# Performance work log

Measured on AMD Instinct MI355X. Metric: run time of the kernel, lower is better.

Reference implementation:

```python
import jax, jax.numpy as jnp
import numpy as np

N = 50000
E = 600000
D_IN = 128
HID = 128
OUT = 64


def setup_inputs() -> dict:
    key = jax.random.key(0)
    ks = jax.random.split(key, 12)
    x = jax.random.normal(ks[0], (N, D_IN), dtype=jnp.float32)
    edge_index = jax.random.randint(ks[1], (2, E), 0, N, dtype=jnp.int32)
    def lin(k, fan_in, fan_out):
        lim = 1.0 / np.sqrt(fan_in)
        kw, kb = jax.random.split(k)
        W = jax.random.uniform(kw, (fan_in, fan_out), minval=-lim, maxval=lim, dtype=jnp.float32)
        b = jax.random.uniform(kb, (fan_out,), minval=-lim, maxval=lim, dtype=jnp.float32)
        return W, b
    W1, b1 = lin(ks[2], D_IN, HID)
    W2, b2 = lin(ks[3], HID, HID)
    W3, b3 = lin(ks[4], HID, HID)
    fcW, fcb = lin(ks[5], HID, OUT)
    return {"x": x, "edge_index": edge_index, "W1": W1, "b1": b1,
            "W2": W2, "b2": b2, "W3": W3, "b3": b3, "fcW": fcW, "fcb": fcb}


def _gcn_prep(edge_index):
    # add self loops, compute symmetric normalization deg^-1/2 * deg^-1/2
    loop = jnp.arange(N, dtype=edge_index.dtype)
    src = jnp.concatenate([edge_index[0], loop])
    dst = jnp.concatenate([edge_index[1], loop])
    deg = jax.ops.segment_sum(jnp.ones_like(dst, dtype=jnp.float32), dst, num_segments=N)
    dinv = jnp.where(deg > 0, jax.lax.rsqrt(deg), 0.0)
    norm = dinv[src] * dinv[dst]  # [E+N]
    return src, dst, norm


def _gcn_layer(x, src, dst, norm, W, b):
    h = x @ W                      # [N, F_out]
    msg = h[src] * norm[:, None]   # gather + scale, [E+N, F_out]
    agg = jax.ops.segment_sum(msg, dst, num_segments=N)
    return agg + b


def reference(x, edge_index, W1, b1, W2, b2, W3, b3, fcW, fcb):
    src, dst, norm = _gcn_prep(edge_index)
    x = jax.nn.relu(_gcn_layer(x, src, dst, norm, W1, b1))
    x = jax.nn.relu(_gcn_layer(x, src, dst, norm, W2, b2))
    x = jax.nn.relu(_gcn_layer(x, src, dst, norm, W3, b3))
    virtual_node_embedding = x[-1]  # last node's embedding [HID]
    out = virtual_node_embedding @ fcW + fcb  # [OUT]
    return out
```

## Files before the change

kernel.cpp:

```cpp
#include <hip/hip_runtime.h>

#define NF 128
#define OUTF 64

#define M2 1
#define M1 2
#define M0 4

#define CAP_F2 2048
#define CAP_E3 4096
#define CAP_F1 32768
#define CAP_E2 65536
#define CAP_F0 131072
#define CAP_E1 262144


__global__ void k_seed(int* __restrict__ mark, int* __restrict__ F2,
                       int* __restrict__ cnt, int last) {
    if (threadIdx.x == 0) {
        mark[last] = M2;
        F2[0] = last;
        cnt[0] = 1;
    }
}

__global__ void k_mark(const int* __restrict__ src, const int* __restrict__ dst, int E,
                       int* __restrict__ mark, int checkBit, int setBit, int last,
                       int2* __restrict__ Elist, int Ecap, int* __restrict__ eCnt,
                       int* __restrict__ Flist, int Fcap, int* __restrict__ fCnt,
                       const int* __restrict__ selfList, const int* __restrict__ selfCnt,
                       int selfCap)
{
    int i = blockIdx.x * blockDim.x + threadIdx.x;

    if (selfList) {
        int sc = *selfCnt; if (sc > selfCap) sc = selfCap;
        if (i < sc) {
            int v = selfList[i];
            if (!(atomicOr(&mark[v], setBit) & setBit)) {
                int p = atomicAdd(fCnt, 1);
                if (p < Fcap) Flist[p] = v;
            }
        }
    }
    if (i < E) {
        int d = dst[i];
        bool hit = checkBit ? ((mark[d] & checkBit) != 0) : (d == last);
        if (hit) {
            int s = src[i];
            int p = atomicAdd(eCnt, 1);
            if (p < Ecap) Elist[p] = make_int2(s, d);
            if (!(atomicOr(&mark[s], setBit) & setBit)) {
                int q = atomicAdd(fCnt, 1);
                if (q < Fcap) Flist[q] = s;
            }
        }
    }
}

__global__ void k_degm(const int* __restrict__ dst, const int* __restrict__ mark,
                       int* __restrict__ deg, int E) {
    int i = blockIdx.x * blockDim.x + threadIdx.x;
    if (i < E) {
        int d = dst[i];
        if (mark[d]) atomicAdd(&deg[d], 1);
    }
}

__global__ void k_dinvm(const int* __restrict__ mark, const int* __restrict__ deg,
                        float* __restrict__ dinv, int n) {
    int i = blockIdx.x * blockDim.x + threadIdx.x;
    if (i < n && mark[i]) dinv[i] = rsqrtf(1.0f + (float)deg[i]);
}

__global__ __launch_bounds__(256) void k_gemm_rows(
    const int* __restrict__ list, const int* __restrict__ cntPtr, int cap,
    const float* __restrict__ Xin, const float* __restrict__ bias,
    const float* __restrict__ W, const float* __restrict__ dinv,
    const int* __restrict__ mark, int aggBit, int last,
    float* __restrict__ H, float* __restrict__ AGG)
{
    __shared__ float wsm[128][128];
    const int t = threadIdx.x;

    {
        const float4* W4 = (const float4*)W;
        float4* S4 = (float4*)&wsm[0][0];
        #pragma unroll
        for (int it = 0; it < 16; ++it) S4[it * 256 + t] = W4[it * 256 + t];
    }
    __syncthreads();

    int cnt = *cntPtr; if (cnt > cap) cnt = cap;
    const int wave = t >> 6, lane = t & 63;

    for (int base = blockIdx.x * 4; base < cnt; base += gridDim.x * 4) {
        int r = base + wave;
        if (r >= cnt) continue;
        int v = list[r];
        size_t off = (size_t)v * NF;

        float x0, x1;
        if (bias) {
            x0 = fmaxf(Xin[off + lane]      + bias[lane],      0.f);
            x1 = fmaxf(Xin[off + lane + 64] + bias[lane + 64], 0.f);
        } else {
            x0 = Xin[off + lane];
            x1 = Xin[off + lane + 64];
        }

        float a0 = 0.f, a1 = 0.f;
        #pragma unroll 16
        for (int k = 0; k < 64; ++k) {
            float xk = __shfl(x0, k);
            a0 += xk * wsm[k][lane];
            a1 += xk * wsm[k][lane + 64];
        }
        #pragma unroll 16
        for (int k = 0; k < 64; ++k) {
            float xk = __shfl(x1, k);
            a0 += xk * wsm[k + 64][lane];
            a1 += xk * wsm[k + 64][lane + 64];
        }

        H[off + lane]      = a0;
        H[off + lane + 64] = a1;

        bool doAgg = (mark ? ((mark[v] & aggBit) != 0) : false) || (v == last);
        if (doAgg) {
            float di = dinv[v], s2 = di * di;
            AGG[off + lane]      = a0 * s2;
            AGG[off + lane + 64] = a1 * s2;
        }
    }
}

__global__ void k_scat(const int2* __restrict__ list, const int* __restrict__ cntPtr, int cap,
                       const float* __restrict__ dinv, const float* __restrict__ H,
                       float* __restrict__ AGG)
{
    int cnt = *cntPtr; if (cnt > cap) cnt = cap;
    int t = threadIdx.x;
    for (int i = blockIdx.x; i < cnt; i += gridDim.x) {
        int2 e = list[i];
        float w = dinv[e.x] * dinv[e.y];
        atomicAdd(&AGG[(size_t)e.y * NF + t], H[(size_t)e.x * NF + t] * w);
    }
}

__global__ void k_fc(const float* __restrict__ AGG3, const float* __restrict__ b3,
                     const float* __restrict__ fcW, const float* __restrict__ fcb,
                     float* __restrict__ out, int last)
{
    __shared__ float xrow[NF];
    int j = threadIdx.x;
    size_t off = (size_t)last * NF;
    xrow[j]      = fmaxf(AGG3[off + j]      + b3[j],      0.f);
    xrow[j + 64] = fmaxf(AGG3[off + j + 64] + b3[j + 64], 0.f);
    __syncthreads();
    float acc = fcb[j];
    #pragma unroll 16
    for (int k = 0; k < NF; ++k) acc += xrow[k] * fcW[k * OUTF + j];
    out[j] = acc;
}

extern "C" void kernel_launch(void* const* d_in, const int* in_sizes, int n_in,
                              void* d_out, int out_size, void* d_ws, size_t ws_size,
                              hipStream_t stream)
{
    const float* x    = (const float*)d_in[0];
    const int*   ei   = (const int*)d_in[1];
    const float* W1   = (const float*)d_in[2];
    const float* b1   = (const float*)d_in[3];
    const float* W2   = (const float*)d_in[4];
    const float* b2   = (const float*)d_in[5];
    const float* W3   = (const float*)d_in[6];
    const float* b3   = (const float*)d_in[7];
    const float* fcW  = (const float*)d_in[8];
    const float* fcb  = (const float*)d_in[9];
    float* out = (float*)d_out;

    const int n = in_sizes[0] / NF;
    const int E = in_sizes[1] / 2;
    const int* src = ei;
    const int* dst = ei + E;
    const int last = n - 1;

    char* wp = (char*)d_ws;
    auto alloc = [&](size_t bytes) -> void* {
        void* r = (void*)wp;
        wp += (bytes + 255) & ~(size_t)255;
        return r;
    };
    int*   deg  = (int*)alloc((size_t)n * 4);
    int*   mark = (int*)alloc((size_t)n * 4);
    int*   cnt  = (int*)alloc(64 * 4);
    size_t zbytes = (char*)wp - (char*)deg;

    float* dinv = (float*)alloc((size_t)n * 4);
    int*   F2   = (int*) alloc(CAP_F2 * 4);
    int2*  E3   = (int2*)alloc(CAP_E3 * 8);
    int*   F1   = (int*) alloc(CAP_F1 * 4);
    int2*  E2   = (int2*)alloc(CAP_E2 * 8);
    int*   F0   = (int*) alloc(CAP_F0 * 4);
    int2*  E1   = (int2*)alloc(CAP_E1 * 8);
    float* H    = (float*)alloc((size_t)n * NF * 4);
    float* aggA = (float*)alloc((size_t)n * NF * 4);
    float* aggB = (float*)alloc((size_t)n * NF * 4);

    const int B  = 256;
    const int EB = (E + B - 1) / B;
    const int NB = (n + B - 1) / B;

    hipMemsetAsync(deg, 0, zbytes, stream);
    k_seed<<<1, 64, 0, stream>>>(mark, F2, cnt, last);

    k_mark<<<EB, B, 0, stream>>>(src, dst, E, mark, 0,  M2, last,
                                 E3, CAP_E3, &cnt[1], F2, CAP_F2, &cnt[0],
                                 nullptr, nullptr, 0);
    k_mark<<<EB, B, 0, stream>>>(src, dst, E, mark, M2, M1, last,
                                 E2, CAP_E2, &cnt[3], F1, CAP_F1, &cnt[2],
                                 F2, &cnt[0], CAP_F2);
    k_mark<<<EB, B, 0, stream>>>(src, dst, E, mark, M1, M0, last,
                                 E1, CAP_E1, &cnt[5], F0, CAP_F0, &cnt[4],
                                 F1, &cnt[2], CAP_F1);

    k_degm <<<EB, B, 0, stream>>>(dst, mark, deg, E);
    k_dinvm<<<NB, B, 0, stream>>>(mark, deg, dinv, n);

    k_gemm_rows<<<384, B, 0, stream>>>(F0, &cnt[4], CAP_F0, x, nullptr, W1,
                                       dinv, mark, M1, -1, H, aggA);
    k_scat<<<2048, 128, 0, stream>>>(E1, &cnt[5], CAP_E1, dinv, H, aggA);

    k_gemm_rows<<<384, B, 0, stream>>>(F1, &cnt[2], CAP_F1, aggA, b1, W2,
                                       dinv, mark, M2, -1, H, aggB);
    k_scat<<<2048, 128, 0, stream>>>(E2, &cnt[3], CAP_E2, dinv, H, aggB);

    k_gemm_rows<<<384, B, 0, stream>>>(F2, &cnt[0], CAP_F2, aggB, b2, W3,
                                       dinv, nullptr, 0, last, H, aggA);
    k_scat<<<2048, 128, 0, stream>>>(E3, &cnt[1], CAP_E3, dinv, H, aggA);

    k_fc<<<1, 64, 0, stream>>>(aggA, b3, fcW, fcb, out, last);
}
```

Measured before the change: 167.8 us.

## Fuse all GCN stages into one cooperative persistent kernel with grid syncs

Replaces about twelve separate launches (memset, seed, three mark passes, degree, dinv, three gemm and scatter pairs, fc) with a single cooperative kernel of 256 blocks that separates phases with grid.sync. Degree counting is folded into the first edge pass and dinv is recomputed on the fly from deg instead of being stored. The aim is to remove launch overhead and inter-kernel gaps. In exchange, parallelism is capped at 256 blocks, every phase pays a grid-wide barrier, and degree atomics now run for all edges rather than only marked destinations.

```diff
diff --git a/kernel.cpp b/kernel.cpp
--- a/kernel.cpp
+++ b/kernel.cpp
@@ -1,4 +1,7 @@
 #include <hip/hip_runtime.h>
+#include <hip/hip_cooperative_groups.h>
+
+namespace cg = cooperative_groups;
 
 #define NF 128
 #define OUTF 64
@@ -15,176 +18,201 @@
 #define CAP_E1 262144
 
 
-__global__ void k_seed(int* __restrict__ mark, int* __restrict__ F2,
-                       int* __restrict__ cnt, int last) {
-    if (threadIdx.x == 0) {
-        mark[last] = M2;
-        F2[0] = last;
-        cnt[0] = 1;
-    }
+struct Params {
+    const float* x; const int* src; const int* dst; int E; int n; int last;
+    const float* W1; const float* b1; const float* W2; const float* b2;
+    const float* W3; const float* b3; const float* fcW; const float* fcb;
+    int* deg; int* mark; int* cnt;
+    int* F2; int2* E3l; int* F1; int2* E2l; int* F0; int2* E1l;
+    float* H; float* aggA; float* aggB; float* out;
+};
+
+__device__ __forceinline__ float dinv_of(const int* deg, int v) {
+    return rsqrtf(1.0f + (float)deg[v]);
 }
 
-__global__ void k_mark(const int* __restrict__ src, const int* __restrict__ dst, int E,
-                       int* __restrict__ mark, int checkBit, int setBit, int last,
-                       int2* __restrict__ Elist, int Ecap, int* __restrict__ eCnt,
-                       int* __restrict__ Flist, int Fcap, int* __restrict__ fCnt,
-                       const int* __restrict__ selfList, const int* __restrict__ selfCnt,
-                       int selfCap)
-{
-    int i = blockIdx.x * blockDim.x + threadIdx.x;
-
-    if (selfList) {
-        int sc = *selfCnt; if (sc > selfCap) sc = selfCap;
-        if (i < sc) {
-            int v = selfList[i];
-            if (!(atomicOr(&mark[v], setBit) & setBit)) {
-                int p = atomicAdd(fCnt, 1);
-                if (p < Fcap) Flist[p] = v;
-            }
-        }
-    }
-    if (i < E) {
-        int d = dst[i];
-        bool hit = checkBit ? ((mark[d] & checkBit) != 0) : (d == last);
-        if (hit) {
-            int s = src[i];
-            int p = atomicAdd(eCnt, 1);
-            if (p < Ecap) Elist[p] = make_int2(s, d);
-            if (!(atomicOr(&mark[s], setBit) & setBit)) {
-                int q = atomicAdd(fCnt, 1);
-                if (q < Fcap) Flist[q] = s;
-            }
-        }
-    }
-}
-
-__global__ void k_degm(const int* __restrict__ dst, const int* __restrict__ mark,
-                       int* __restrict__ deg, int E) {
-    int i = blockIdx.x * blockDim.x + threadIdx.x;
-    if (i < E) {
-        int d = dst[i];
-        if (mark[d]) atomicAdd(&deg[d], 1);
-    }
-}
-
-__global__ void k_dinvm(const int* __restrict__ mark, const int* __restrict__ deg,
-                        float* __restrict__ dinv, int n) {
-    int i = blockIdx.x * blockDim.x + threadIdx.x;
-    if (i < n && mark[i]) dinv[i] = rsqrtf(1.0f + (float)deg[i]);
-}
-
-__global__ __launch_bounds__(256) void k_gemm_rows(
-    const int* __restrict__ list, const int* __restrict__ cntPtr, int cap,
-    const float* __restrict__ Xin, const float* __restrict__ bias,
-    const float* __restrict__ W, const float* __restrict__ dinv,
-    const int* __restrict__ mark, int aggBit, int last,
-    float* __restrict__ H, float* __restrict__ AGG)
-{
+__global__ __launch_bounds__(256) void k_fused(Params p) {
+    cg::grid_group grid = cg::this_grid();
     __shared__ float wsm[128][128];
-    const int t = threadIdx.x;
+
+    const int t       = threadIdx.x;
+    const int gtid    = blockIdx.x * 256 + t;
+    const int gstride = gridDim.x * 256;
+    const int last    = p.last;
+
+    for (int i = gtid; i < p.n; i += gstride) {
+        p.deg[i]  = 0;
+        p.mark[i] = (i == last) ? M2 : 0;
+    }
+    if (gtid < 64) p.cnt[gtid] = (gtid == 0) ? 1 : 0;
+    if (gtid == 0) p.F2[0] = last;
+    grid.sync();
+
+    for (int i = gtid; i < p.E; i += gstride) {
+        int d = p.dst[i];
+        atomicAdd(&p.deg[d], 1);
+        if (d == last) {
+            int s = p.src[i];
+            int pe = atomicAdd(&p.cnt[1], 1);
+            if (pe < CAP_E3) p.E3l[pe] = make_int2(s, d);
+            if (!(atomicOr(&p.mark[s], M2) & M2)) {
+                int q = atomicAdd(&p.cnt[0], 1);
+                if (q < CAP_F2) p.F2[q] = s;
+            }
+        }
+    }
+    grid.sync();
 
     {
-        const float4* W4 = (const float4*)W;
+        int sc = p.cnt[0]; if (sc > CAP_F2) sc = CAP_F2;
+        for (int i = gtid; i < sc; i += gstride) {
+            int v = p.F2[i];
+            if (!(atomicOr(&p.mark[v], M1) & M1)) {
+                int q = atomicAdd(&p.cnt[2], 1);
+                if (q < CAP_F1) p.F1[q] = v;
+            }
+        }
+        for (int i = gtid; i < p.E; i += gstride) {
+            int d = p.dst[i];
+            if (p.mark[d] & M2) {
+                int s = p.src[i];
+                int pe = atomicAdd(&p.cnt[3], 1);
+                if (pe < CAP_E2) p.E2l[pe] = make_int2(s, d);
+                if (!(atomicOr(&p.mark[s], M1) & M1)) {
+                    int q = atomicAdd(&p.cnt[2], 1);
+                    if (q < CAP_F1) p.F1[q] = s;
+                }
+            }
+        }
+    }
+    grid.sync();
+
+    {
+        int sc = p.cnt[2]; if (sc > CAP_F1) sc = CAP_F1;
+        for (int i = gtid; i < sc; i += gstride) {
+            int v = p.F1[i];
+            if (!(atomicOr(&p.mark[v], M0) & M0)) {
+                int q = atomicAdd(&p.cnt[4], 1);
+                if (q < CAP_F0) p.F0[q] = v;
+            }
+        }
+        for (int i = gtid; i < p.E; i += gstride) {
+            int d = p.dst[i];
+            if (p.mark[d] & M1) {
+                int s = p.src[i];
+                int pe = atomicAdd(&p.cnt[5], 1);
+                if (pe < CAP_E1) p.E1l[pe] = make_int2(s, d);
+                if (!(atomicOr(&p.mark[s], M0) & M0)) {
+                    int q = atomicAdd(&p.cnt[4], 1);
+                    if (q < CAP_F0) p.F0[q] = s;
+                }
+            }
+        }
+    }
+    grid.sync();
+
+    int cF2 = p.cnt[0]; if (cF2 > CAP_F2) cF2 = CAP_F2;
+    int cE3 = p.cnt[1]; if (cE3 > CAP_E3) cE3 = CAP_E3;
+    int cF1 = p.cnt[2]; if (cF1 > CAP_F1) cF1 = CAP_F1;
+    int cE2 = p.cnt[3]; if (cE2 > CAP_E2) cE2 = CAP_E2;
+    int cF0 = p.cnt[4]; if (cF0 > CAP_F0) cF0 = CAP_F0;
+    int cE1 = p.cnt[5]; if (cE1 > CAP_E1) cE1 = CAP_E1;
+
+    const int wave = t >> 6, lane = t & 63;
+
+    auto gemm = [&](const int* list, int cntv, const float* Xin, const float* bias,
+                    const float* Wg, int aggBit, float* H, float* AGG) {
+        const float4* W4 = (const float4*)Wg;
         float4* S4 = (float4*)&wsm[0][0];
         #pragma unroll
         for (int it = 0; it < 16; ++it) S4[it * 256 + t] = W4[it * 256 + t];
-    }
-    __syncthreads();
-
-    int cnt = *cntPtr; if (cnt > cap) cnt = cap;
-    const int wave = t >> 6, lane = t & 63;
-
-    for (int base = blockIdx.x * 4; base < cnt; base += gridDim.x * 4) {
-        int r = base + wave;
-        if (r >= cnt) continue;
-        int v = list[r];
-        size_t off = (size_t)v * NF;
-
-        float x0, x1;
-        if (bias) {
-            x0 = fmaxf(Xin[off + lane]      + bias[lane],      0.f);
-            x1 = fmaxf(Xin[off + lane + 64] + bias[lane + 64], 0.f);
-        } else {
-            x0 = Xin[off + lane];
-            x1 = Xin[off + lane + 64];
-        }
-
-        float a0 = 0.f, a1 = 0.f;
-        #pragma unroll 16
-        for (int k = 0; k < 64; ++k) {
-            float xk = __shfl(x0, k);
-            a0 += xk * wsm[k][lane];
-            a1 += xk * wsm[k][lane + 64];
-        }
-        #pragma unroll 16
-        for (int k = 0; k < 64; ++k) {
-            float xk = __shfl(x1, k);
-            a0 += xk * wsm[k + 64][lane];
-            a1 += xk * wsm[k + 64][lane + 64];
-        }
-
-        H[off + lane]      = a0;
-        H[off + lane + 64] = a1;
-
-        bool doAgg = (mark ? ((mark[v] & aggBit) != 0) : false) || (v == last);
-        if (doAgg) {
-            float di = dinv[v], s2 = di * di;
-            AGG[off + lane]      = a0 * s2;
-            AGG[off + lane + 64] = a1 * s2;
-        }
-    }
-}
-
-__global__ void k_scat(const int2* __restrict__ list, const int* __restrict__ cntPtr, int cap,
-                       const float* __restrict__ dinv, const float* __restrict__ H,
-                       float* __restrict__ AGG)
-{
-    int cnt = *cntPtr; if (cnt > cap) cnt = cap;
-    int t = threadIdx.x;
-    for (int i = blockIdx.x; i < cnt; i += gridDim.x) {
-        int2 e = list[i];
-        float w = dinv[e.x] * dinv[e.y];
-        atomicAdd(&AGG[(size_t)e.y * NF + t], H[(size_t)e.x * NF + t] * w);
-    }
-}
-
-__global__ void k_fc(const float* __restrict__ AGG3, const float* __restrict__ b3,
-                     const float* __restrict__ fcW, const float* __restrict__ fcb,
-                     float* __restrict__ out, int last)
-{
-    __shared__ float xrow[NF];
-    int j = threadIdx.x;
-    size_t off = (size_t)last * NF;
-    xrow[j]      = fmaxf(AGG3[off + j]      + b3[j],      0.f);
-    xrow[j + 64] = fmaxf(AGG3[off + j + 64] + b3[j + 64], 0.f);
-    __syncthreads();
-    float acc = fcb[j];
-    #pragma unroll 16
-    for (int k = 0; k < NF; ++k) acc += xrow[k] * fcW[k * OUTF + j];
-    out[j] = acc;
+        __syncthreads();
+
+        for (int r = blockIdx.x * 4 + wave; r < cntv; r += gridDim.x * 4) {
+            int v = list[r];
+            size_t off = (size_t)v * NF;
+            float x0, x1;
+            if (bias) {
+                x0 = fmaxf(Xin[off + lane]      + bias[lane],      0.f);
+                x1 = fmaxf(Xin[off + lane + 64] + bias[lane + 64], 0.f);
+            } else {
+                x0 = Xin[off + lane];
+                x1 = Xin[off + lane + 64];
+            }
+            float a0 = 0.f, a1 = 0.f;
+            #pragma unroll 16
+            for (int k = 0; k < 64; ++k) {
+                float xk = __shfl(x0, k);
+                a0 += xk * wsm[k][lane];
+                a1 += xk * wsm[k][lane + 64];
+            }
+            #pragma unroll 16
+            for (int k = 0; k < 64; ++k) {
+                float xk = __shfl(x1, k);
+                a0 += xk * wsm[k + 64][lane];
+                a1 += xk * wsm[k + 64][lane + 64];
+            }
+            H[off + lane]      = a0;
+            H[off + lane + 64] = a1;
+
+            bool doAgg = aggBit ? ((p.mark[v] & aggBit) != 0) : (v == last);
+            if (doAgg) {
+                float di = dinv_of(p.deg, v);
+                float s2 = di * di;
+                AGG[off + lane]      = a0 * s2;
+                AGG[off + lane + 64] = a1 * s2;
+            }
+        }
+    };
+
+    auto scat = [&](const int2* El, int ec, const float* H, float* AGG) {
+        int half = t >> 7;
+        int f    = t & 127;
+        for (int i = blockIdx.x * 2 + half; i < ec; i += gridDim.x * 2) {
+            int2 e = El[i];
+            float w = dinv_of(p.deg, e.x) * dinv_of(p.deg, e.y);
+            atomicAdd(&AGG[(size_t)e.y * NF + f], H[(size_t)e.x * NF + f] * w);
+        }
+    };
+
+    gemm(p.F0, cF0, p.x, nullptr, p.W1, M1, p.H, p.aggA);
+    grid.sync();
+    scat(p.E1l, cE1, p.H, p.aggA);
+    grid.sync();
+
+    gemm(p.F1, cF1, p.aggA, p.b1, p.W2, M2, p.H, p.aggB);
+    grid.sync();
+    scat(p.E2l, cE2, p.H, p.aggB);
+    grid.sync();
+
+    gemm(p.F2, cF2, p.aggB, p.b2, p.W3, 0, p.H, p.aggA);
+    grid.sync();
+    scat(p.E3l, cE3, p.H, p.aggA);
+    grid.sync();
+
+    if (blockIdx.x == 0) {
+        float* xrow = &wsm[0][0];
+        size_t off = (size_t)last * NF;
+        if (t < 64) {
+            xrow[t]      = fmaxf(p.aggA[off + t]      + p.b3[t],      0.f);
+            xrow[t + 64] = fmaxf(p.aggA[off + t + 64] + p.b3[t + 64], 0.f);
+        }
+        __syncthreads();
+        if (t < 64) {
+            float acc = p.fcb[t];
+            #pragma unroll 16
+            for (int k = 0; k < NF; ++k) acc += xrow[k] * p.fcW[k * OUTF + t];
+            p.out[t] = acc;
+        }
+    }
 }
 
 extern "C" void kernel_launch(void* const* d_in, const int* in_sizes, int n_in,
                               void* d_out, int out_size, void* d_ws, size_t ws_size,
                               hipStream_t stream)
 {
-    const float* x    = (const float*)d_in[0];
-    const int*   ei   = (const int*)d_in[1];
-    const float* W1   = (const float*)d_in[2];
-    const float* b1   = (const float*)d_in[3];
-    const float* W2   = (const float*)d_in[4];
-    const float* b2   = (const float*)d_in[5];
-    const float* W3   = (const float*)d_in[6];
-    const float* b3   = (const float*)d_in[7];
-    const float* fcW  = (const float*)d_in[8];
-    const float* fcb  = (const float*)d_in[9];
-    float* out = (float*)d_out;
-
     const int n = in_sizes[0] / NF;
     const int E = in_sizes[1] / 2;
-    const int* src = ei;
-    const int* dst = ei + E;
-    const int last = n - 1;
 
     char* wp = (char*)d_ws;
     auto alloc = [&](size_t bytes) -> void* {
@@ -192,53 +220,38 @@
         wp += (bytes + 255) & ~(size_t)255;
         return r;
     };
-    int*   deg  = (int*)alloc((size_t)n * 4);
-    int*   mark = (int*)alloc((size_t)n * 4);
-    int*   cnt  = (int*)alloc(64 * 4);
-    size_t zbytes = (char*)wp - (char*)deg;
-
-    float* dinv = (float*)alloc((size_t)n * 4);
-    int*   F2   = (int*) alloc(CAP_F2 * 4);
-    int2*  E3   = (int2*)alloc(CAP_E3 * 8);
-    int*   F1   = (int*) alloc(CAP_F1 * 4);
-    int2*  E2   = (int2*)alloc(CAP_E2 * 8);
-    int*   F0   = (int*) alloc(CAP_F0 * 4);
-    int2*  E1   = (int2*)alloc(CAP_E1 * 8);
-    float* H    = (float*)alloc((size_t)n * NF * 4);
-    float* aggA = (float*)alloc((size_t)n * NF * 4);
-    float* aggB = (float*)alloc((size_t)n * NF * 4);
-
-    const int B  = 256;
-    const int EB = (E + B - 1) / B;
-    const int NB = (n + B - 1) / B;
-
-    hipMemsetAsync(deg, 0, zbytes, stream);
-    k_seed<<<1, 64, 0, stream>>>(mark, F2, cnt, last);
-
-    k_mark<<<EB, B, 0, stream>>>(src, dst, E, mark, 0,  M2, last,
-                                 E3, CAP_E3, &cnt[1], F2, CAP_F2, &cnt[0],
-                                 nullptr, nullptr, 0);
-    k_mark<<<EB, B, 0, stream>>>(src, dst, E, mark, M2, M1, last,
-                                 E2, CAP_E2, &cnt[3], F1, CAP_F1, &cnt[2],
-                                 F2, &cnt[0], CAP_F2);
-    k_mark<<<EB, B, 0, stream>>>(src, dst, E, mark, M1, M0, last,
-                                 E1, CAP_E1, &cnt[5], F0, CAP_F0, &cnt[4],
-                                 F1, &cnt[2], CAP_F1);
-
-    k_degm <<<EB, B, 0, stream>>>(dst, mark, deg, E);
-    k_dinvm<<<NB, B, 0, stream>>>(mark, deg, dinv, n);
-
-    k_gemm_rows<<<384, B, 0, stream>>>(F0, &cnt[4], CAP_F0, x, nullptr, W1,
-                                       dinv, mark, M1, -1, H, aggA);
-    k_scat<<<2048, 128, 0, stream>>>(E1, &cnt[5], CAP_E1, dinv, H, aggA);
-
-    k_gemm_rows<<<384, B, 0, stream>>>(F1, &cnt[2], CAP_F1, aggA, b1, W2,
-                                       dinv, mark, M2, -1, H, aggB);
-    k_scat<<<2048, 128, 0, stream>>>(E2, &cnt[3], CAP_E2, dinv, H, aggB);
-
-    k_gemm_rows<<<384, B, 0, stream>>>(F2, &cnt[0], CAP_F2, aggB, b2, W3,
-                                       dinv, nullptr, 0, last, H, aggA);
-    k_scat<<<2048, 128, 0, stream>>>(E3, &cnt[1], CAP_E3, dinv, H, aggA);
-
-    k_fc<<<1, 64, 0, stream>>>(aggA, b3, fcW, fcb, out, last);
+
+    Params p;
+    p.x    = (const float*)d_in[0];
+    p.src  = (const int*)d_in[1];
+    p.dst  = (const int*)d_in[1] + E;
+    p.E    = E;
+    p.n    = n;
+    p.last = n - 1;
+    p.W1   = (const float*)d_in[2];
+    p.b1   = (const float*)d_in[3];
+    p.W2   = (const float*)d_in[4];
+    p.b2   = (const float*)d_in[5];
+    p.W3   = (const float*)d_in[6];
+    p.b3   = (const float*)d_in[7];
+    p.fcW  = (const float*)d_in[8];
+    p.fcb  = (const float*)d_in[9];
+
+    p.deg  = (int*)  alloc((size_t)n * 4);
+    p.mark = (int*)  alloc((size_t)n * 4);
+    p.cnt  = (int*)  alloc(64 * 4);
+    p.F2   = (int*)  alloc(CAP_F2 * 4);
+    p.E3l  = (int2*) alloc(CAP_E3 * 8);
+    p.F1   = (int*)  alloc(CAP_F1 * 4);
+    p.E2l  = (int2*) alloc(CAP_E2 * 8);
+    p.F0   = (int*)  alloc(CAP_F0 * 4);
+    p.E1l  = (int2*) alloc(CAP_E1 * 8);
+    p.H    = (float*)alloc((size_t)n * NF * 4);
+    p.aggA = (float*)alloc((size_t)n * NF * 4);
+    p.aggB = (float*)alloc((size_t)n * NF * 4);
+    p.out  = (float*)d_out;
+
+    void* args[] = { &p };
+    hipLaunchCooperativeKernel((const void*)k_fused, dim3(256), dim3(256),
+                               args, 0, stream);
 }
```

Result: slower. 447.1 us (+166.4%).
